# Kernel optimization log

Measured on AMD Instinct MI355X. Metric: run time of the kernel, lower is better.

Reference implementation:

```python
import jax, jax.numpy as jnp
import numpy as np

B, S, H, MI, E, K, SI = 4, 1024, 1024, 512, 16, 2, 2048


def setup_inputs() -> dict:
    key = jax.random.key(0)
    ks = jax.random.split(key, 8)
    s = 0.02  # weight scale ~ glorot-ish
    return {
        "hidden_states": jax.random.normal(ks[0], (B, S, H), jnp.float32),
        "router_w": jax.random.normal(ks[1], (H, E), jnp.float32) * s,
        "expert_gate_up_w": jax.random.normal(ks[2], (E, H, 2 * MI), jnp.float32) * s,
        "expert_down_w": jax.random.normal(ks[3], (E, MI, H), jnp.float32) * s,
        "shared_gate_w": jax.random.normal(ks[4], (H, SI), jnp.float32) * s,
        "shared_up_w": jax.random.normal(ks[5], (H, SI), jnp.float32) * s,
        "shared_down_w": jax.random.normal(ks[6], (SI, H), jnp.float32) * s,
        "shared_expert_gate_w": jax.random.normal(ks[7], (H, 1), jnp.float32) * s,
    }


def reference(hidden_states, router_w, expert_gate_up_w, expert_down_w,
              shared_gate_w, shared_up_w, shared_down_w, shared_expert_gate_w):
    b, s, h = hidden_states.shape
    x = hidden_states.reshape(-1, h)  # [T, H]
    T = x.shape[0]

    # Shared expert: SwiGLU MLP gated by sigmoid(shared_expert_gate)
    g = jax.nn.silu(x @ shared_gate_w)          # [T, SI]
    u = x @ shared_up_w                          # [T, SI]
    shared_out = (u * g) @ shared_down_w         # [T, H]
    shared_out = jax.nn.sigmoid(x @ shared_expert_gate_w) * shared_out

    # Router: softmax -> top-k -> renormalize -> dense [T, E] routing weights
    router_logits = x @ router_w                 # [T, E]
    probs = jax.nn.softmax(router_logits, axis=-1)
    top_p, top_i = jax.lax.top_k(probs, K)       # [T, K]
    top_p = top_p / jnp.sum(top_p, axis=-1, keepdims=True)
    routing = jnp.zeros((T, probs.shape[-1]), x.dtype).at[
        jnp.arange(T)[:, None], top_i].add(top_p)  # [T, E]

    # All-experts SwiGLU (compute-all-then-select, as in source)
    gate_up = jnp.einsum('th,ehm->etm', x, expert_gate_up_w)  # [E, T, 2*MI]
    gate, up = jnp.split(gate_up, 2, axis=-1)
    hidden = up * jax.nn.silu(gate)                            # [E, T, MI]
    expert_out = jnp.einsum('eti,eih->eth', hidden, expert_down_w)  # [E, T, H]
    contrib = jnp.einsum('eth,te->th', expert_out, routing)    # [T, H]

    out = (contrib + shared_out).reshape(b, s, h)
    return out, router_logits
```

## Files before the change

kernel.cpp:

```cpp
#include <hip/hip_runtime.h>
#include <hip/hip_bf16.h>
#include <cstdint>

#define T_  4096
#define H_  1024
#define E_  16
#define MI_ 512
#define SI_ 2048
#define TK_ 8192

typedef __bf16 bf16;
typedef bf16  bf16x8 __attribute__((ext_vector_type(8)));
typedef bf16  bf16x4 __attribute__((ext_vector_type(4)));
typedef float f32x4  __attribute__((ext_vector_type(4)));

__device__ __forceinline__ void gload16(const bf16* g, bf16* lds) {
    __builtin_amdgcn_global_load_lds(
        (const __attribute__((address_space(1))) void*)(uintptr_t)(const void*)g,
        (__attribute__((address_space(3))) void*)(uintptr_t)(void*)lds,
        16, 0, 0);
}

__global__ void k_convert(const float* __restrict__ src, bf16* __restrict__ dst, int n4) {
    int i = blockIdx.x * blockDim.x + threadIdx.x;
    if (i < n4) {
        float4 v = reinterpret_cast<const float4*>(src)[i];
        bf16x4 o;
        o[0] = (bf16)v.x; o[1] = (bf16)v.y; o[2] = (bf16)v.z; o[3] = (bf16)v.w;
        reinterpret_cast<bf16x4*>(dst)[i] = o;
    }
}

__global__ void k_transpose(const float* __restrict__ src, bf16* __restrict__ dst, int R, int C) {
    __shared__ float tile[32][33];
    size_t zoff = (size_t)blockIdx.z * (size_t)R * (size_t)C;
    src += zoff; dst += zoff;
    int c  = blockIdx.x * 32 + threadIdx.x;
    #pragma unroll
    for (int i = 0; i < 4; i++) {
        int r = blockIdx.y * 32 + threadIdx.y + i * 8;
        tile[threadIdx.y + i * 8][threadIdx.x] = src[(size_t)r * C + c];
    }
    __syncthreads();
    int rr = blockIdx.y * 32 + threadIdx.x;
    #pragma unroll
    for (int i = 0; i < 4; i++) {
        int cc = blockIdx.x * 32 + threadIdx.y + i * 8;
        dst[(size_t)cc * R + rr] = (bf16)tile[threadIdx.x][threadIdx.y + i * 8];
    }
}

__global__ __launch_bounds__(256) void k_router(
    const float* __restrict__ x, const float* __restrict__ rw,
    const float* __restrict__ segw, float* __restrict__ logits_out,
    int* __restrict__ top_i, float* __restrict__ top_w,
    float* __restrict__ gate_scalar)
{
    int wid = threadIdx.x >> 6, lane = threadIdx.x & 63;
    int t = blockIdx.x * 4 + wid;
    const float* xr = x + (size_t)t * H_;
    float acc[E_];
    #pragma unroll
    for (int e = 0; e < E_; e++) acc[e] = 0.f;
    float accg = 0.f;
    for (int j = 0; j < H_ / 64; j++) {
        int h = j * 64 + lane;
        float xv = xr[h];
        const float4* wrow = reinterpret_cast<const float4*>(rw + (size_t)h * E_);
        #pragma unroll
        for (int q = 0; q < 4; q++) {
            float4 w4 = wrow[q];
            acc[q*4+0] += xv * w4.x; acc[q*4+1] += xv * w4.y;
            acc[q*4+2] += xv * w4.z; acc[q*4+3] += xv * w4.w;
        }
        accg += xv * segw[h];
    }
    #pragma unroll
    for (int off = 32; off >= 1; off >>= 1) {
        #pragma unroll
        for (int e = 0; e < E_; e++) acc[e] += __shfl_xor(acc[e], off);
        accg += __shfl_xor(accg, off);
    }
    if (lane == 0) {
        float* lo = logits_out + (size_t)t * E_;
        #pragma unroll
        for (int e = 0; e < E_; e++) lo[e] = acc[e];
        int i0 = 0; float l0 = acc[0];
        #pragma unroll
        for (int e = 1; e < E_; e++) if (acc[e] > l0) { l0 = acc[e]; i0 = e; }
        int i1 = -1; float l1 = -1e30f;
        #pragma unroll
        for (int e = 0; e < E_; e++) if (e != i0 && acc[e] > l1) { l1 = acc[e]; i1 = e; }
        float w0 = 1.f / (1.f + expf(l1 - l0));
        top_i[t*2] = i0; top_i[t*2+1] = i1;
        top_w[t*2] = w0; top_w[t*2+1] = 1.f - w0;
        gate_scalar[t] = 1.f / (1.f + expf(-accg));
    }
}

__global__ __launch_bounds__(256) void k_count(const int* __restrict__ top_i, int* __restrict__ offsets) {
    __shared__ int hist[256][17];
    int tid = threadIdx.x;
    #pragma unroll
    for (int e = 0; e < E_; e++) hist[tid][e] = 0;
    __syncthreads();
    const int* mine = top_i + tid * 32;
    #pragma unroll
    for (int j = 0; j < 32; j++) hist[tid][mine[j]]++;
    __syncthreads();
    if (tid < E_) {
        int s = 0;
        for (int r = 0; r < 256; r++) s += hist[r][tid];
        hist[0][tid] = s;
    }
    __syncthreads();
    if (tid == 0) {
        int s = 0;
        for (int e = 0; e < E_; e++) { offsets[e] = s; s += hist[0][e]; }
        offsets[E_] = s;
    }
}

__global__ __launch_bounds__(256) void k_fillscan(
    const int* __restrict__ top_i, const int* __restrict__ offsets,
    int* __restrict__ slot_token, int* __restrict__ slot_pos)
{
    int e = blockIdx.x;
    int tid = threadIdx.x;
    int lane = tid & 63, w = tid >> 6;
    __shared__ int wsum[4];

    int t0 = tid * 16;
    unsigned f0 = 0, f1 = 0;
    int c = 0;
    #pragma unroll
    for (int j = 0; j < 16; j++) {
        int t = t0 + j;
        int a = top_i[t*2], b = top_i[t*2+1];
        if (a == e)      { f0 |= 1u << j; c++; }
        else if (b == e) { f1 |= 1u << j; c++; }
    }
    int incl = c;
    #pragma unroll
    for (int off = 1; off < 64; off <<= 1) {
        int v = __shfl_up(incl, off);
        if (lane >= off) incl += v;
    }
    if (lane == 63) wsum[w] = incl;
    __syncthreads();
    int wbase = 0;
    for (int i = 0; i < w; i++) wbase += wsum[i];
    int pos = offsets[e] + wbase + (incl - c);
    #pragma unroll
    for (int j = 0; j < 16; j++) {
        int t = t0 + j;
        if ((f0 >> j) & 1u)      { slot_token[pos] = t; slot_pos[t*2]   = pos; pos++; }
        else if ((f1 >> j) & 1u) { slot_token[pos] = t; slot_pos[t*2+1] = pos; pos++; }
    }
}

__global__ __launch_bounds__(256) void k_mlp1(
    const bf16* __restrict__ xb, const bf16* __restrict__ wgu,
    const bf16* __restrict__ wsg, const bf16* __restrict__ wsu,
    const int* __restrict__ slot_token, const int* __restrict__ offsets,
    bf16* __restrict__ hiddenE, bf16* __restrict__ sh_hid)
{
    int bid = blockIdx.x;
    bool expert = bid < 4096;
    int nt, mt, base, cnt;
    const bf16 *Bg, *Bu;
    bf16* outp; int nout;
    if (expert) {
        int e = bid >> 8; int r = bid & 255; nt = r & 7; mt = r >> 3;
        base = offsets[e]; cnt = offsets[e+1] - base;
        if (mt * 128 >= cnt) return;
        const bf16* wb = wgu + (size_t)e * (2 * MI_) * H_;
        Bg = wb + (size_t)(nt * 64) * H_;
        Bu = wb + (size_t)(MI_ + nt * 64) * H_;
        outp = hiddenE; nout = MI_;
    } else {
        int r = bid - 4096; nt = r & 31; mt = r >> 5;
        base = 0; cnt = T_;
        Bg = wsg + (size_t)(nt * 64) * H_;
        Bu = wsu + (size_t)(nt * 64) * H_;
        outp = sh_hid; nout = SI_;
    }

    __shared__ __align__(16) bf16 As0[128 * 64], Bs0[128 * 64];
    __shared__ __align__(16) bf16 As1[128 * 64], Bs1[128 * 64];

    int tid = threadIdx.x, w = tid >> 6, l = tid & 63;
    int lrow8 = l >> 3;
    int col_off = ((l & 7) ^ lrow8) * 8;

    const bf16* asrc[4];
    const bf16* bsrc[4];
    #pragma unroll
    for (int g = 0; g < 4; g++) {
        int rt = g * 32 + w * 8 + lrow8;
        int s = mt * 128 + rt; if (s >= cnt) s = cnt - 1;
        asrc[g] = (expert ? xb + (size_t)slot_token[base + s] * H_
                          : xb + (size_t)s * H_) + col_off;
        int half = (rt >> 5) & 1;
        int gcol = ((rt >> 6) << 5) | (rt & 31);
        bsrc[g] = (half ? Bu : Bg) + (size_t)gcol * H_ + col_off;
    }

    int lr = l & 15, kq = l >> 4;
    int wm = w & 1, wn = w >> 1;
    f32x4 acc[4][4];
    #pragma unroll
    for (int mi = 0; mi < 4; mi++)
        #pragma unroll
        for (int ni = 0; ni < 4; ni++) acc[mi][ni] = (f32x4){0.f, 0.f, 0.f, 0.f};

    auto STAGE = [&](bf16* Ad, bf16* Bd, int k0) {
        #pragma unroll
        for (int g = 0; g < 4; g++) {
            gload16(asrc[g] + k0, Ad + (g * 32 + w * 8) * 64);
            gload16(bsrc[g] + k0, Bd + (g * 32 + w * 8) * 64);
        }
    };
    auto COMPUTE = [&](const bf16* Ab, const bf16* Bb) {
        #pragma unroll
        for (int ks = 0; ks < 2; ks++) {
            int cl = ((ks * 4 + kq) ^ (lr & 7)) * 8;
            bf16x8 af[4], bfr[4];
            #pragma unroll
            for (int mi = 0; mi < 4; mi++)
                af[mi] = *reinterpret_cast<const bf16x8*>(&Ab[(wm * 64 + mi * 16 + lr) * 64 + cl]);
            #pragma unroll
            for (int ni = 0; ni < 4; ni++)
                bfr[ni] = *reinterpret_cast<const bf16x8*>(&Bb[(wn * 64 + ni * 16 + lr) * 64 + cl]);
            #pragma unroll
            for (int mi = 0; mi < 4; mi++)
                #pragma unroll
                for (int ni = 0; ni < 4; ni++)
                    acc[mi][ni] = __builtin_amdgcn_mfma_f32_16x16x32_bf16(af[mi], bfr[ni], acc[mi][ni], 0, 0, 0);
        }
    };

    STAGE(As0, Bs0, 0);
    __syncthreads();
    for (int k0 = 0; k0 < H_; k0 += 128) {
        STAGE(As1, Bs1, k0 + 64);
        COMPUTE(As0, Bs0);
        __syncthreads();
        if (k0 + 128 < H_) STAGE(As0, Bs0, k0 + 128);
        COMPUTE(As1, Bs1);
        __syncthreads();
    }

    #pragma unroll
    for (int mi = 0; mi < 4; mi++)
        #pragma unroll
        for (int ni = 0; ni < 2; ni++)
            #pragma unroll
            for (int r = 0; r < 4; r++) {
                int row = mt * 128 + wm * 64 + mi * 16 + kq * 4 + r;
                if (row < cnt) {
                    int col = nt * 64 + wn * 32 + ni * 16 + lr;
                    float g = acc[mi][ni][r], u = acc[mi][ni + 2][r];
                    float hv = u * (g / (1.f + expf(-g)));
                    outp[(size_t)(base + row) * nout + col] = (bf16)hv;
                }
            }
}

__global__ __launch_bounds__(256) void k_mlp2(
    const bf16* __restrict__ hiddenE, const bf16* __restrict__ sh_hid,
    const bf16* __restrict__ wdn, const bf16* __restrict__ wsd,
    const int* __restrict__ offsets, const float* __restrict__ gate_s,
    bf16* __restrict__ eo, float* __restrict__ out)
{
    int bid = blockIdx.x;
    bool expert = bid < 4096;
    int nt, mt, base, cnt, KD;
    const bf16 *Ab, *B0;
    if (expert) {
        int e = bid >> 8; int r = bid & 255; nt = r & 7; mt = r >> 3;
        base = offsets[e]; cnt = offsets[e+1] - base;
        if (mt * 128 >= cnt) return;
        KD = MI_;
        Ab = hiddenE;
        B0 = wdn + (size_t)e * H_ * MI_ + (size_t)(nt * 128) * MI_;
    } else {
        int r = bid - 4096; nt = r & 7; mt = r >> 3;
        base = 0; cnt = T_; KD = SI_;
        Ab = sh_hid;
        B0 = wsd + (size_t)(nt * 128) * SI_;
    }

    __shared__ __align__(16) bf16 As0[128 * 64], Bs0[128 * 64];
    __shared__ __align__(16) bf16 As1[128 * 64], Bs1[128 * 64];

    int tid = threadIdx.x, w = tid >> 6, l = tid & 63;
    int lrow8 = l >> 3;
    int col_off = ((l & 7) ^ lrow8) * 8;

    const bf16* asrc[4];
    const bf16* bsrc[4];
    #pragma unroll
    for (int g = 0; g < 4; g++) {
        int rt = g * 32 + w * 8 + lrow8;
        int s = mt * 128 + rt; if (s >= cnt) s = cnt - 1;
        asrc[g] = Ab + (size_t)(base + s) * KD + col_off;
        bsrc[g] = B0 + (size_t)rt * KD + col_off;
    }

    int lr = l & 15, kq = l >> 4;
    int wm = w & 1, wn = w >> 1;
    f32x4 acc[4][4];
    #pragma unroll
    for (int mi = 0; mi < 4; mi++)
        #pragma unroll
        for (int ni = 0; ni < 4; ni++) acc[mi][ni] = (f32x4){0.f, 0.f, 0.f, 0.f};

    auto STAGE = [&](bf16* Ad, bf16* Bd, int k0) {
        #pragma unroll
        for (int g = 0; g < 4; g++) {
            gload16(asrc[g] + k0, Ad + (g * 32 + w * 8) * 64);
            gload16(bsrc[g] + k0, Bd + (g * 32 + w * 8) * 64);
        }
    };
    auto COMPUTE = [&](const bf16* Abuf, const bf16* Bbuf) {
        #pragma unroll
        for (int ks = 0; ks < 2; ks++) {
            int cl = ((ks * 4 + kq) ^ (lr & 7)) * 8;
            bf16x8 af[4], bfr[4];
            #pragma unroll
            for (int mi = 0; mi < 4; mi++)
                af[mi] = *reinterpret_cast<const bf16x8*>(&Abuf[(wm * 64 + mi * 16 + lr) * 64 + cl]);
            #pragma unroll
            for (int ni = 0; ni < 4; ni++)
                bfr[ni] = *reinterpret_cast<const bf16x8*>(&Bbuf[(wn * 64 + ni * 16 + lr) * 64 + cl]);
            #pragma unroll
            for (int mi = 0; mi < 4; mi++)
                #pragma unroll
                for (int ni = 0; ni < 4; ni++)
                    acc[mi][ni] = __builtin_amdgcn_mfma_f32_16x16x32_bf16(af[mi], bfr[ni], acc[mi][ni], 0, 0, 0);
        }
    };

    STAGE(As0, Bs0, 0);
    __syncthreads();
    for (int k0 = 0; k0 < KD; k0 += 128) {
        STAGE(As1, Bs1, k0 + 64);
        COMPUTE(As0, Bs0);
        __syncthreads();
        if (k0 + 128 < KD) STAGE(As0, Bs0, k0 + 128);
        COMPUTE(As1, Bs1);
        __syncthreads();
    }

    #pragma unroll
    for (int mi = 0; mi < 4; mi++)
        #pragma unroll
        for (int ni = 0; ni < 4; ni++)
            #pragma unroll
            for (int r = 0; r < 4; r++) {
                int row = mt * 128 + wm * 64 + mi * 16 + kq * 4 + r;
                if (row < cnt) {
                    int col = nt * 128 + wn * 64 + ni * 16 + lr;
                    float v = acc[mi][ni][r];
                    if (expert) eo[(size_t)(base + row) * H_ + col] = (bf16)v;
                    else        out[(size_t)row * H_ + col] = gate_s[row] * v;
                }
            }
}

__global__ void k_combine(float* __restrict__ out, const bf16* __restrict__ eo,
                          const int* __restrict__ slot_pos, const float* __restrict__ top_w)
{
    int i = blockIdx.x * blockDim.x + threadIdx.x;
    int t = i >> 8;
    int q = (i & 255) * 4;
    int s0 = slot_pos[t*2], s1 = slot_pos[t*2+1];
    float w0 = top_w[t*2], w1 = top_w[t*2+1];
    bf16x4 e0 = *reinterpret_cast<const bf16x4*>(eo + (size_t)s0 * H_ + q);
    bf16x4 e1 = *reinterpret_cast<const bf16x4*>(eo + (size_t)s1 * H_ + q);
    float4* op = reinterpret_cast<float4*>(out) + i;
    float4 so = *op;
    float4 r;
    r.x = so.x + w0 * (float)e0[0] + w1 * (float)e1[0];
    r.y = so.y + w0 * (float)e0[1] + w1 * (float)e1[1];
    r.z = so.z + w0 * (float)e0[2] + w1 * (float)e1[2];
    r.w = so.w + w0 * (float)e0[3] + w1 * (float)e1[3];
    *op = r;
}

extern "C" void kernel_launch(void* const* d_in, const int* in_sizes, int n_in,
                              void* d_out, int out_size, void* d_ws, size_t ws_size,
                              hipStream_t stream) {
    const float* x    = (const float*)d_in[0];
    const float* rw   = (const float*)d_in[1];
    const float* wgu  = (const float*)d_in[2];
    const float* wdn  = (const float*)d_in[3];
    const float* wsg  = (const float*)d_in[4];
    const float* wsu  = (const float*)d_in[5];
    const float* wsd  = (const float*)d_in[6];
    const float* segw = (const float*)d_in[7];
    float* out    = (float*)d_out;
    float* logits = (float*)d_out + (size_t)T_ * H_;

    char* p = (char*)d_ws;
    bf16* xb      = (bf16*)p;  p += (size_t)T_ * H_ * 2;
    bf16* w_guT   = (bf16*)p;  p += (size_t)E_ * H_ * (2*MI_) * 2;
    bf16* w_dnT   = (bf16*)p;  p += (size_t)E_ * MI_ * H_ * 2;
    bf16* w_sgT   = (bf16*)p;  p += (size_t)H_ * SI_ * 2;
    bf16* w_suT   = (bf16*)p;  p += (size_t)H_ * SI_ * 2;
    bf16* w_sdT   = (bf16*)p;  p += (size_t)SI_ * H_ * 2;
    bf16* hiddenE = (bf16*)p;  p += (size_t)TK_ * MI_ * 2;
    bf16* sh_hid  = (bf16*)p;  p += (size_t)T_ * SI_ * 2;
    bf16* eo      = (bf16*)p;  p += (size_t)TK_ * H_ * 2;
    float* gate_s = (float*)p; p += (size_t)T_ * 4;
    int*  top_i   = (int*)p;   p += (size_t)T_ * 2 * 4;
    float* top_w  = (float*)p; p += (size_t)T_ * 2 * 4;
    int*  slot_pos= (int*)p;   p += (size_t)T_ * 2 * 4;
    int*  slot_tok= (int*)p;   p += (size_t)TK_ * 4;
    int*  offsets = (int*)p;   p += 17 * 4;

    k_convert<<<dim3(T_*H_/4/256), 256, 0, stream>>>(x, xb, T_*H_/4);
    k_transpose<<<dim3(32, 32, 16), dim3(32, 8), 0, stream>>>(wgu, w_guT, 1024, 1024);
    k_transpose<<<dim3(32, 16, 16), dim3(32, 8), 0, stream>>>(wdn, w_dnT, 512, 1024);
    k_transpose<<<dim3(64, 32, 1),  dim3(32, 8), 0, stream>>>(wsg, w_sgT, 1024, 2048);
    k_transpose<<<dim3(64, 32, 1),  dim3(32, 8), 0, stream>>>(wsu, w_suT, 1024, 2048);
    k_transpose<<<dim3(32, 64, 1),  dim3(32, 8), 0, stream>>>(wsd, w_sdT, 2048, 1024);

    k_router<<<dim3(T_/4), 256, 0, stream>>>(x, rw, segw, logits, top_i, top_w, gate_s);
    k_count<<<dim3(1), 256, 0, stream>>>(top_i, offsets);
    k_fillscan<<<dim3(E_), 256, 0, stream>>>(top_i, offsets, slot_tok, slot_pos);

    k_mlp1<<<dim3(4096 + 1024), 256, 0, stream>>>(xb, w_guT, w_sgT, w_suT, slot_tok, offsets, hiddenE, sh_hid);
    k_mlp2<<<dim3(4096 + 256), 256, 0, stream>>>(hiddenE, sh_hid, w_dnT, w_sdT, offsets, gate_s, eo, out);

    k_combine<<<dim3(T_*256/256), 256, 0, stream>>>(out, eo, slot_pos, top_w);
}
```

Measured before the change: 220.2 us.

## Deepen GEMM pipeline to four LDS stages with partial vmcnt waits and block remap

Result: slower. 442.6 us (+101.0%).

```diff
diff --git a/kernel.cpp b/kernel.cpp
--- a/kernel.cpp
+++ b/kernel.cpp
@@ -20,6 +20,13 @@
         (__attribute__((address_space(3))) void*)(uintptr_t)(void*)lds,
         16, 0, 0);
 }
+
+#define PIPE_BAR(N) do {                                                    \
+    __builtin_amdgcn_sched_barrier(0);                                      \
+    asm volatile("s_waitcnt vmcnt(" #N ") lgkmcnt(0)" ::: "memory");        \
+    __builtin_amdgcn_s_barrier();                                           \
+    __builtin_amdgcn_sched_barrier(0);                                      \
+} while (0)
 
 __global__ void k_convert(const float* __restrict__ src, bf16* __restrict__ dst, int n4) {
     int i = blockIdx.x * blockDim.x + threadIdx.x;
@@ -165,7 +172,7 @@
     const int* __restrict__ slot_token, const int* __restrict__ offsets,
     bf16* __restrict__ hiddenE, bf16* __restrict__ sh_hid)
 {
-    int bid = blockIdx.x;
+    int bid = (blockIdx.x & 7) * 640 + (blockIdx.x >> 3);
     bool expert = bid < 4096;
     int nt, mt, base, cnt;
     const bf16 *Bg, *Bu;
@@ -186,18 +193,20 @@
         outp = sh_hid; nout = SI_;
     }
 
-    __shared__ __align__(16) bf16 As0[128 * 64], Bs0[128 * 64];
-    __shared__ __align__(16) bf16 As1[128 * 64], Bs1[128 * 64];
+    __shared__ __align__(16) bf16 A0[128*32], Bq0[128*32];
+    __shared__ __align__(16) bf16 A1[128*32], Bq1[128*32];
+    __shared__ __align__(16) bf16 A2[128*32], Bq2[128*32];
+    __shared__ __align__(16) bf16 A3[128*32], Bq3[128*32];
 
     int tid = threadIdx.x, w = tid >> 6, l = tid & 63;
-    int lrow8 = l >> 3;
-    int col_off = ((l & 7) ^ lrow8) * 8;
-
-    const bf16* asrc[4];
-    const bf16* bsrc[4];
-    #pragma unroll
-    for (int g = 0; g < 4; g++) {
-        int rt = g * 32 + w * 8 + lrow8;
+    int lrow = l >> 2;
+    int col_off = ((l & 3) ^ ((l >> 3) & 3)) * 8;
+
+    const bf16* asrc[2];
+    const bf16* bsrc[2];
+    #pragma unroll
+    for (int g = 0; g < 2; g++) {
+        int rt = g * 64 + w * 16 + lrow;
         int s = mt * 128 + rt; if (s >= cnt) s = cnt - 1;
         asrc[g] = (expert ? xb + (size_t)slot_token[base + s] * H_
                           : xb + (size_t)s * H_) + col_off;
@@ -215,41 +224,39 @@
         for (int ni = 0; ni < 4; ni++) acc[mi][ni] = (f32x4){0.f, 0.f, 0.f, 0.f};
 
     auto STAGE = [&](bf16* Ad, bf16* Bd, int k0) {
-        #pragma unroll
-        for (int g = 0; g < 4; g++) {
-            gload16(asrc[g] + k0, Ad + (g * 32 + w * 8) * 64);
-            gload16(bsrc[g] + k0, Bd + (g * 32 + w * 8) * 64);
-        }
+        gload16(asrc[0] + k0, Ad + (w * 16) * 32);
+        gload16(asrc[1] + k0, Ad + (64 + w * 16) * 32);
+        gload16(bsrc[0] + k0, Bd + (w * 16) * 32);
+        gload16(bsrc[1] + k0, Bd + (64 + w * 16) * 32);
     };
     auto COMPUTE = [&](const bf16* Ab, const bf16* Bb) {
-        #pragma unroll
-        for (int ks = 0; ks < 2; ks++) {
-            int cl = ((ks * 4 + kq) ^ (lr & 7)) * 8;
-            bf16x8 af[4], bfr[4];
-            #pragma unroll
-            for (int mi = 0; mi < 4; mi++)
-                af[mi] = *reinterpret_cast<const bf16x8*>(&Ab[(wm * 64 + mi * 16 + lr) * 64 + cl]);
+        int cl = (kq ^ ((lr >> 1) & 3)) * 8;
+        bf16x8 af[4], bfr[4];
+        #pragma unroll
+        for (int mi = 0; mi < 4; mi++)
+            af[mi] = *reinterpret_cast<const bf16x8*>(&Ab[(wm * 64 + mi * 16 + lr) * 32 + cl]);
+        #pragma unroll
+        for (int ni = 0; ni < 4; ni++)
+            bfr[ni] = *reinterpret_cast<const bf16x8*>(&Bb[(wn * 64 + ni * 16 + lr) * 32 + cl]);
+        #pragma unroll
+        for (int mi = 0; mi < 4; mi++)
             #pragma unroll
             for (int ni = 0; ni < 4; ni++)
-                bfr[ni] = *reinterpret_cast<const bf16x8*>(&Bb[(wn * 64 + ni * 16 + lr) * 64 + cl]);
-            #pragma unroll
-            for (int mi = 0; mi < 4; mi++)
-                #pragma unroll
-                for (int ni = 0; ni < 4; ni++)
-                    acc[mi][ni] = __builtin_amdgcn_mfma_f32_16x16x32_bf16(af[mi], bfr[ni], acc[mi][ni], 0, 0, 0);
-        }
+                acc[mi][ni] = __builtin_amdgcn_mfma_f32_16x16x32_bf16(af[mi], bfr[ni], acc[mi][ni], 0, 0, 0);
     };
 
-    STAGE(As0, Bs0, 0);
-    __syncthreads();
-    for (int k0 = 0; k0 < H_; k0 += 128) {
-        STAGE(As1, Bs1, k0 + 64);
-        COMPUTE(As0, Bs0);
-        __syncthreads();
-        if (k0 + 128 < H_) STAGE(As0, Bs0, k0 + 128);
-        COMPUTE(As1, Bs1);
-        __syncthreads();
-    }
+    STAGE(A0, Bq0, 0); STAGE(A1, Bq1, 32); STAGE(A2, Bq2, 64);
+    PIPE_BAR(8);
+    for (int kb = 0; kb + 256 <= H_; kb += 128) {
+        STAGE(A3, Bq3, kb +  96); COMPUTE(A0, Bq0); PIPE_BAR(8);
+        STAGE(A0, Bq0, kb + 128); COMPUTE(A1, Bq1); PIPE_BAR(8);
+        STAGE(A1, Bq1, kb + 160); COMPUTE(A2, Bq2); PIPE_BAR(8);
+        STAGE(A2, Bq2, kb + 192); COMPUTE(A3, Bq3); PIPE_BAR(8);
+    }
+    STAGE(A3, Bq3, H_ - 32); COMPUTE(A0, Bq0); PIPE_BAR(8);
+    COMPUTE(A1, Bq1); PIPE_BAR(4);
+    COMPUTE(A2, Bq2); PIPE_BAR(0);
+    COMPUTE(A3, Bq3);
 
     #pragma unroll
     for (int mi = 0; mi < 4; mi++)
@@ -273,7 +280,7 @@
     const int* __restrict__ offsets, const float* __restrict__ gate_s,
     bf16* __restrict__ eo, float* __restrict__ out)
 {
-    int bid = blockIdx.x;
+    int bid = (blockIdx.x & 7) * 544 + (blockIdx.x >> 3);
     bool expert = bid < 4096;
     int nt, mt, base, cnt, KD;
     const bf16 *Ab, *B0;
@@ -291,18 +298,20 @@
         B0 = wsd + (size_t)(nt * 128) * SI_;
     }
 
-    __shared__ __align__(16) bf16 As0[128 * 64], Bs0[128 * 64];
-    __shared__ __align__(16) bf16 As1[128 * 64], Bs1[128 * 64];
+    __shared__ __align__(16) bf16 A0[128*32], Bq0[128*32];
+    __shared__ __align__(16) bf16 A1[128*32], Bq1[128*32];
+    __shared__ __align__(16) bf16 A2[128*32], Bq2[128*32];
+    __shared__ __align__(16) bf16 A3[128*32], Bq3[128*32];
 
     int tid = threadIdx.x, w = tid >> 6, l = tid & 63;
-    int lrow8 = l >> 3;
-    int col_off = ((l & 7) ^ lrow8) * 8;
-
-    const bf16* asrc[4];
-    const bf16* bsrc[4];
-    #pragma unroll
-    for (int g = 0; g < 4; g++) {
-        int rt = g * 32 + w * 8 + lrow8;
+    int lrow = l >> 2;
+    int col_off = ((l & 3) ^ ((l >> 3) & 3)) * 8;
+
+    const bf16* asrc[2];
+    const bf16* bsrc[2];
+    #pragma unroll
+    for (int g = 0; g < 2; g++) {
+        int rt = g * 64 + w * 16 + lrow;
         int s = mt * 128 + rt; if (s >= cnt) s = cnt - 1;
         asrc[g] = Ab + (size_t)(base + s) * KD + col_off;
         bsrc[g] = B0 + (size_t)rt * KD + col_off;
@@ -317,41 +326,39 @@
         for (int ni = 0; ni < 4; ni++) acc[mi][ni] = (f32x4){0.f, 0.f, 0.f, 0.f};
 
     auto STAGE = [&](bf16* Ad, bf16* Bd, int k0) {
-        #pragma unroll
-        for (int g = 0; g < 4; g++) {
-            gload16(asrc[g] + k0, Ad + (g * 32 + w * 8) * 64);
-            gload16(bsrc[g] + k0, Bd + (g * 32 + w * 8) * 64);
-        }
+        gload16(asrc[0] + k0, Ad + (w * 16) * 32);
+        gload16(asrc[1] + k0, Ad + (64 + w * 16) * 32);
+        gload16(bsrc[0] + k0, Bd + (w * 16) * 32);
+        gload16(bsrc[1] + k0, Bd + (64 + w * 16) * 32);
     };
-    auto COMPUTE = [&](const bf16* Abuf, const bf16* Bbuf) {
-        #pragma unroll
-        for (int ks = 0; ks < 2; ks++) {
-            int cl = ((ks * 4 + kq) ^ (lr & 7)) * 8;
-            bf16x8 af[4], bfr[4];
-            #pragma unroll
-            for (int mi = 0; mi < 4; mi++)
-                af[mi] = *reinterpret_cast<const bf16x8*>(&Abuf[(wm * 64 + mi * 16 + lr) * 64 + cl]);
+    auto COMPUTE = [&](const bf16* Abf, const bf16* Bbf) {
+        int cl = (kq ^ ((lr >> 1) & 3)) * 8;
+        bf16x8 af[4], bfr[4];
+        #pragma unroll
+        for (int mi = 0; mi < 4; mi++)
+            af[mi] = *reinterpret_cast<const bf16x8*>(&Abf[(wm * 64 + mi * 16 + lr) * 32 + cl]);
+        #pragma unroll
+        for (int ni = 0; ni < 4; ni++)
+            bfr[ni] = *reinterpret_cast<const bf16x8*>(&Bbf[(wn * 64 + ni * 16 + lr) * 32 + cl]);
+        #pragma unroll
+        for (int mi = 0; mi < 4; mi++)
             #pragma unroll
             for (int ni = 0; ni < 4; ni++)
-                bfr[ni] = *reinterpret_cast<const bf16x8*>(&Bbuf[(wn * 64 + ni * 16 + lr) * 64 + cl]);
-            #pragma unroll
-            for (int mi = 0; mi < 4; mi++)
-                #pragma unroll
-                for (int ni = 0; ni < 4; ni++)
-                    acc[mi][ni] = __builtin_amdgcn_mfma_f32_16x16x32_bf16(af[mi], bfr[ni], acc[mi][ni], 0, 0, 0);
-        }
+                acc[mi][ni] = __builtin_amdgcn_mfma_f32_16x16x32_bf16(af[mi], bfr[ni], acc[mi][ni], 0, 0, 0);
     };
 
-    STAGE(As0, Bs0, 0);
-    __syncthreads();
-    for (int k0 = 0; k0 < KD; k0 += 128) {
-        STAGE(As1, Bs1, k0 + 64);
-        COMPUTE(As0, Bs0);
-        __syncthreads();
-        if (k0 + 128 < KD) STAGE(As0, Bs0, k0 + 128);
-        COMPUTE(As1, Bs1);
-        __syncthreads();
-    }
+    STAGE(A0, Bq0, 0); STAGE(A1, Bq1, 32); STAGE(A2, Bq2, 64);
+    PIPE_BAR(8);
+    for (int kb = 0; kb + 256 <= KD; kb += 128) {
+        STAGE(A3, Bq3, kb +  96); COMPUTE(A0, Bq0); PIPE_BAR(8);
+        STAGE(A0, Bq0, kb + 128); COMPUTE(A1, Bq1); PIPE_BAR(8);
+        STAGE(A1, Bq1, kb + 160); COMPUTE(A2, Bq2); PIPE_BAR(8);
+        STAGE(A2, Bq2, kb + 192); COMPUTE(A3, Bq3); PIPE_BAR(8);
+    }
+    STAGE(A3, Bq3, KD - 32); COMPUTE(A0, Bq0); PIPE_BAR(8);
+    COMPUTE(A1, Bq1); PIPE_BAR(4);
+    COMPUTE(A2, Bq2); PIPE_BAR(0);
+    COMPUTE(A3, Bq3);
 
     #pragma unroll
     for (int mi = 0; mi < 4; mi++)
```

## Use 256-row M tiles with 512-thread blocks and XCD-aware block remap in MLP GEMMs

Applied to the files above, without the earlier changes.

New measurement: 412.5 us. 1.87x slower.

```diff
diff --git a/kernel.cpp b/kernel.cpp
--- a/kernel.cpp
+++ b/kernel.cpp
@@ -159,55 +159,59 @@
     }
 }
 
-__global__ __launch_bounds__(256) void k_mlp1(
+__global__ __launch_bounds__(512) void k_mlp1(
     const bf16* __restrict__ xb, const bf16* __restrict__ wgu,
     const bf16* __restrict__ wsg, const bf16* __restrict__ wsu,
     const int* __restrict__ slot_token, const int* __restrict__ offsets,
     bf16* __restrict__ hiddenE, bf16* __restrict__ sh_hid)
 {
-    int bid = blockIdx.x;
-    bool expert = bid < 4096;
+    int bid = (blockIdx.x & 7) * 320 + (blockIdx.x >> 3);
+    bool expert = bid < 2048;
     int nt, mt, base, cnt;
     const bf16 *Bg, *Bu;
     bf16* outp; int nout;
     if (expert) {
-        int e = bid >> 8; int r = bid & 255; nt = r & 7; mt = r >> 3;
+        int e = bid >> 7; int r = bid & 127; nt = r & 7; mt = r >> 3;
         base = offsets[e]; cnt = offsets[e+1] - base;
-        if (mt * 128 >= cnt) return;
+        if (mt * 256 >= cnt) return;
         const bf16* wb = wgu + (size_t)e * (2 * MI_) * H_;
         Bg = wb + (size_t)(nt * 64) * H_;
         Bu = wb + (size_t)(MI_ + nt * 64) * H_;
         outp = hiddenE; nout = MI_;
     } else {
-        int r = bid - 4096; nt = r & 31; mt = r >> 5;
+        int r = bid - 2048; nt = r & 31; mt = r >> 5;
         base = 0; cnt = T_;
         Bg = wsg + (size_t)(nt * 64) * H_;
         Bu = wsu + (size_t)(nt * 64) * H_;
         outp = sh_hid; nout = SI_;
     }
 
-    __shared__ __align__(16) bf16 As0[128 * 64], Bs0[128 * 64];
-    __shared__ __align__(16) bf16 As1[128 * 64], Bs1[128 * 64];
+    __shared__ __align__(16) bf16 A0[256 * 64], B0s[128 * 64];
+    __shared__ __align__(16) bf16 A1[256 * 64], B1s[128 * 64];
 
     int tid = threadIdx.x, w = tid >> 6, l = tid & 63;
-    int lrow8 = l >> 3;
-    int col_off = ((l & 7) ^ lrow8) * 8;
+    int rg = l >> 3;
+    int col_off = ((l & 7) ^ rg) * 8;
 
     const bf16* asrc[4];
-    const bf16* bsrc[4];
+    const bf16* bsrc[2];
     #pragma unroll
     for (int g = 0; g < 4; g++) {
-        int rt = g * 32 + w * 8 + lrow8;
-        int s = mt * 128 + rt; if (s >= cnt) s = cnt - 1;
+        int rt = g * 64 + w * 8 + rg;
+        int s = mt * 256 + rt; if (s >= cnt) s = cnt - 1;
         asrc[g] = (expert ? xb + (size_t)slot_token[base + s] * H_
                           : xb + (size_t)s * H_) + col_off;
+    }
+    #pragma unroll
+    for (int g = 0; g < 2; g++) {
+        int rt = g * 64 + w * 8 + rg;
         int half = (rt >> 5) & 1;
         int gcol = ((rt >> 6) << 5) | (rt & 31);
         bsrc[g] = (half ? Bu : Bg) + (size_t)gcol * H_ + col_off;
     }
 
     int lr = l & 15, kq = l >> 4;
-    int wm = w & 1, wn = w >> 1;
+    int wm = w & 3, wn = w >> 2;
     f32x4 acc[4][4];
     #pragma unroll
     for (int mi = 0; mi < 4; mi++)
@@ -216,16 +220,17 @@
 
     auto STAGE = [&](bf16* Ad, bf16* Bd, int k0) {
         #pragma unroll
-        for (int g = 0; g < 4; g++) {
-            gload16(asrc[g] + k0, Ad + (g * 32 + w * 8) * 64);
-            gload16(bsrc[g] + k0, Bd + (g * 32 + w * 8) * 64);
-        }
+        for (int g = 0; g < 4; g++)
+            gload16(asrc[g] + k0, Ad + (g * 64 + w * 8) * 64);
+        #pragma unroll
+        for (int g = 0; g < 2; g++)
+            gload16(bsrc[g] + k0, Bd + (g * 64 + w * 8) * 64);
     };
     auto COMPUTE = [&](const bf16* Ab, const bf16* Bb) {
         #pragma unroll
         for (int ks = 0; ks < 2; ks++) {
+            bf16x8 af[4], bfr[4];
             int cl = ((ks * 4 + kq) ^ (lr & 7)) * 8;
-            bf16x8 af[4], bfr[4];
             #pragma unroll
             for (int mi = 0; mi < 4; mi++)
                 af[mi] = *reinterpret_cast<const bf16x8*>(&Ab[(wm * 64 + mi * 16 + lr) * 64 + cl]);
@@ -240,14 +245,14 @@
         }
     };
 
-    STAGE(As0, Bs0, 0);
+    STAGE(A0, B0s, 0);
     __syncthreads();
     for (int k0 = 0; k0 < H_; k0 += 128) {
-        STAGE(As1, Bs1, k0 + 64);
-        COMPUTE(As0, Bs0);
+        STAGE(A1, B1s, k0 + 64);
+        COMPUTE(A0, B0s);
         __syncthreads();
-        if (k0 + 128 < H_) STAGE(As0, Bs0, k0 + 128);
-        COMPUTE(As1, Bs1);
+        if (k0 + 128 < H_) STAGE(A0, B0s, k0 + 128);
+        COMPUTE(A1, B1s);
         __syncthreads();
     }
 
@@ -257,7 +262,7 @@
         for (int ni = 0; ni < 2; ni++)
             #pragma unroll
             for (int r = 0; r < 4; r++) {
-                int row = mt * 128 + wm * 64 + mi * 16 + kq * 4 + r;
+                int row = mt * 256 + wm * 64 + mi * 16 + kq * 4 + r;
                 if (row < cnt) {
                     int col = nt * 64 + wn * 32 + ni * 16 + lr;
                     float g = acc[mi][ni][r], u = acc[mi][ni + 2][r];
@@ -267,49 +272,53 @@
             }
 }
 
-__global__ __launch_bounds__(256) void k_mlp2(
+__global__ __launch_bounds__(512) void k_mlp2(
     const bf16* __restrict__ hiddenE, const bf16* __restrict__ sh_hid,
     const bf16* __restrict__ wdn, const bf16* __restrict__ wsd,
     const int* __restrict__ offsets, const float* __restrict__ gate_s,
     bf16* __restrict__ eo, float* __restrict__ out)
 {
-    int bid = blockIdx.x;
-    bool expert = bid < 4096;
+    int bid = (blockIdx.x & 7) * 272 + (blockIdx.x >> 3);
+    bool expert = bid < 2048;
     int nt, mt, base, cnt, KD;
-    const bf16 *Ab, *B0;
+    const bf16 *Ab, *Bb;
     if (expert) {
-        int e = bid >> 8; int r = bid & 255; nt = r & 7; mt = r >> 3;
+        int e = bid >> 7; int r = bid & 127; nt = r & 7; mt = r >> 3;
         base = offsets[e]; cnt = offsets[e+1] - base;
-        if (mt * 128 >= cnt) return;
+        if (mt * 256 >= cnt) return;
         KD = MI_;
         Ab = hiddenE;
-        B0 = wdn + (size_t)e * H_ * MI_ + (size_t)(nt * 128) * MI_;
+        Bb = wdn + (size_t)e * H_ * MI_ + (size_t)(nt * 128) * MI_;
     } else {
-        int r = bid - 4096; nt = r & 7; mt = r >> 3;
+        int r = bid - 2048; nt = r & 7; mt = r >> 3;
         base = 0; cnt = T_; KD = SI_;
         Ab = sh_hid;
-        B0 = wsd + (size_t)(nt * 128) * SI_;
-    }
-
-    __shared__ __align__(16) bf16 As0[128 * 64], Bs0[128 * 64];
-    __shared__ __align__(16) bf16 As1[128 * 64], Bs1[128 * 64];
+        Bb = wsd + (size_t)(nt * 128) * SI_;
+    }
+
+    __shared__ __align__(16) bf16 A0[256 * 64], B0s[128 * 64];
+    __shared__ __align__(16) bf16 A1[256 * 64], B1s[128 * 64];
 
     int tid = threadIdx.x, w = tid >> 6, l = tid & 63;
-    int lrow8 = l >> 3;
-    int col_off = ((l & 7) ^ lrow8) * 8;
+    int rg = l >> 3;
+    int col_off = ((l & 7) ^ rg) * 8;
 
     const bf16* asrc[4];
-    const bf16* bsrc[4];
+    const bf16* bsrc[2];
     #pragma unroll
     for (int g = 0; g < 4; g++) {
-        int rt = g * 32 + w * 8 + lrow8;
-        int s = mt * 128 + rt; if (s >= cnt) s = cnt - 1;
+        int rt = g * 64 + w * 8 + rg;
+        int s = mt * 256 + rt; if (s >= cnt) s = cnt - 1;
         asrc[g] = Ab + (size_t)(base + s) * KD + col_off;
-        bsrc[g] = B0 + (size_t)rt * KD + col_off;
+    }
+    #pragma unroll
+    for (int g = 0; g < 2; g++) {
+        int rt = g * 64 + w * 8 + rg;
+        bsrc[g] = Bb + (size_t)rt * KD + col_off;
     }
 
     int lr = l & 15, kq = l >> 4;
-    int wm = w & 1, wn = w >> 1;
+    int wm = w & 3, wn = w >> 2;
     f32x4 acc[4][4];
     #pragma unroll
     for (int mi = 0; mi < 4; mi++)
@@ -318,22 +327,23 @@
 
     auto STAGE = [&](bf16* Ad, bf16* Bd, int k0) {
         #pragma unroll
-        for (int g = 0; g < 4; g++) {
-            gload16(asrc[g] + k0, Ad + (g * 32 + w * 8) * 64);
-            gload16(bsrc[g] + k0, Bd + (g * 32 + w * 8) * 64);
-        }
+        for (int g = 0; g < 4; g++)
+            gload16(asrc[g] + k0, Ad + (g * 64 + w * 8) * 64);
+        #pragma unroll
+        for (int g = 0; g < 2; g++)
+            gload16(bsrc[g] + k0, Bd + (g * 64 + w * 8) * 64);
     };
-    auto COMPUTE = [&](const bf16* Abuf, const bf16* Bbuf) {
+    auto COMPUTE = [&](const bf16* Abf, const bf16* Bbf) {
         #pragma unroll
         for (int ks = 0; ks < 2; ks++) {
+            bf16x8 af[4], bfr[4];
             int cl = ((ks * 4 + kq) ^ (lr & 7)) * 8;
-            bf16x8 af[4], bfr[4];
             #pragma unroll
             for (int mi = 0; mi < 4; mi++)
-                af[mi] = *reinterpret_cast<const bf16x8*>(&Abuf[(wm * 64 + mi * 16 + lr) * 64 + cl]);
+                af[mi] = *reinterpret_cast<const bf16x8*>(&Abf[(wm * 64 + mi * 16 + lr) * 64 + cl]);
             #pragma unroll
             for (int ni = 0; ni < 4; ni++)
-                bfr[ni] = *reinterpret_cast<const bf16x8*>(&Bbuf[(wn * 64 + ni * 16 + lr) * 64 + cl]);
+                bfr[ni] = *reinterpret_cast<const bf16x8*>(&Bbf[(wn * 64 + ni * 16 + lr) * 64 + cl]);
             #pragma unroll
             for (int mi = 0; mi < 4; mi++)
                 #pragma unroll
@@ -342,14 +352,14 @@
         }
     };
 
-    STAGE(As0, Bs0, 0);
+    STAGE(A0, B0s, 0);
     __syncthreads();
     for (int k0 = 0; k0 < KD; k0 += 128) {
-        STAGE(As1, Bs1, k0 + 64);
-        COMPUTE(As0, Bs0);
+        STAGE(A1, B1s, k0 + 64);
+        COMPUTE(A0, B0s);
         __syncthreads();
-        if (k0 + 128 < KD) STAGE(As0, Bs0, k0 + 128);
-        COMPUTE(As1, Bs1);
+        if (k0 + 128 < KD) STAGE(A0, B0s, k0 + 128);
+        COMPUTE(A1, B1s);
         __syncthreads();
     }
 
@@ -359,7 +369,7 @@
         for (int ni = 0; ni < 4; ni++)
             #pragma unroll
             for (int r = 0; r < 4; r++) {
-                int row = mt * 128 + wm * 64 + mi * 16 + kq * 4 + r;
+                int row = mt * 256 + wm * 64 + mi * 16 + kq * 4 + r;
                 if (row < cnt) {
                     int col = nt * 128 + wn * 64 + ni * 16 + lr;
                     float v = acc[mi][ni][r];
@@ -431,8 +441,8 @@
     k_count<<<dim3(1), 256, 0, stream>>>(top_i, offsets);
     k_fillscan<<<dim3(E_), 256, 0, stream>>>(top_i, offsets, slot_tok, slot_pos);
 
-    k_mlp1<<<dim3(4096 + 1024), 256, 0, stream>>>(xb, w_guT, w_sgT, w_suT, slot_tok, offsets, hiddenE, sh_hid);
-    k_mlp2<<<dim3(4096 + 256), 256, 0, stream>>>(hiddenE, sh_hid, w_dnT, w_sdT, offsets, gate_s, eo, out);
+    k_mlp1<<<dim3(2048 + 512), 512, 0, stream>>>(xb, w_guT, w_sgT, w_suT, slot_tok, offsets, hiddenE, sh_hid);
+    k_mlp2<<<dim3(2048 + 128), 512, 0, stream>>>(hiddenE, sh_hid, w_dnT, w_sdT, offsets, gate_s, eo, out);
 
     k_combine<<<dim3(T_*256/256), 256, 0, stream>>>(out, eo, slot_pos, top_w);
 }
```
